# Kernel optimization log

Hardware: AMD Instinct MI355X
Metric: run time of the kernel (lower is better)

## Reference

```python
import jax, jax.numpy as jnp
import numpy as np

C = 128          # hidden width hard-coded in DirModelToFace
EPS = 1e-5       # BatchNorm1d eps


def sparse_bmm(rows, cols, vals, x, num_rows):
    """Batched sparse @ dense: COO (rows, cols, vals) shared across batch.
    x: [B, K, c] -> [B, num_rows, c]."""
    def one(xb):
        return jax.ops.segment_sum(xb[cols] * vals[:, None], rows, num_segments=num_rows)
    return jax.vmap(one)(x)


def conv1x1_prebn(x, gamma, beta, W, b):
    # GraphConv1x1(batch_norm='pre'): BN (training stats over B*N rows) then Linear
    mean = x.mean((0, 1))
    var = x.var((0, 1))  # biased, as torch BN uses for normalization
    xh = (x - mean) * jax.lax.rsqrt(var + EPS) * gamma + beta
    return xh @ W + b


def dir_block(Di, DiA, v, f, g, be, W, b):
    # DirResNet2 (res_f=False): quaternionic Dirac message passing
    B, N, _ = v.shape
    Fn = f.shape[1]
    msg_v = sparse_bmm(*DiA, f.reshape(B, 4 * Fn, C // 4), 4 * N).reshape(B, N, C)
    x = jax.nn.elu(jnp.concatenate([v, msg_v], axis=-1))
    v_out = v + conv1x1_prebn(x, g[0], be[0], W[0], b[0])
    msg_f = sparse_bmm(*Di, v_out.reshape(B, 4 * N, C // 4), 4 * Fn).reshape(B, Fn, C)
    x = jax.nn.elu(jnp.concatenate([f, msg_f], axis=-1))
    f_out = conv1x1_prebn(x, g[1], be[1], W[1], b[1])  # no residual on f
    return v_out, f_out


def avg_block(mask, v, g, be, W, b):
    # AvgResNet2: masked global average message
    x = v
    for j in range(2):
        x = jax.nn.elu(x)
        x_avg = (mask * x).sum(1, keepdims=True) / mask.sum(1, keepdims=True)
        x = jnp.concatenate([x, jnp.broadcast_to(x_avg, x.shape)], axis=-1)
        x = conv1x1_prebn(x, g[j], be[j], W[j], b[j])
    return x + v


def setup_inputs() -> dict:
    key = jax.random.key(0)
    ks = jax.random.split(key, 10)
    B, N, Fn = 4, 12000, 24000
    nnz = 48 * Fn  # 3 vertices per face x 4x4 quaternion block
    inputs = jax.random.normal(ks[0], (B, N, 3), jnp.float32)
    mask = jnp.ones((B, N, 1), jnp.float32)
    Di_rows = jax.random.randint(ks[1], (nnz,), 0, 4 * Fn, jnp.int32)
    Di_cols = jax.random.randint(ks[2], (nnz,), 0, 4 * N, jnp.int32)
    Di_vals = jax.random.normal(ks[3], (nnz,), jnp.float32) * 0.1
    DiA_rows = jax.random.randint(ks[4], (nnz,), 0, 4 * N, jnp.int32)
    DiA_cols = jax.random.randint(ks[5], (nnz,), 0, 4 * Fn, jnp.int32)
    DiA_vals = jax.random.normal(ks[6], (nnz,), jnp.float32) * 0.1
    W1 = jax.random.normal(ks[7], (3, C), jnp.float32) / np.sqrt(3.0)
    b1 = jnp.zeros((C,), jnp.float32)
    rn_gamma = jnp.ones((16, 2, 2 * C), jnp.float32)
    rn_beta = jnp.zeros((16, 2, 2 * C), jnp.float32)
    rn_W = jax.random.normal(ks[8], (16, 2, 2 * C, C), jnp.float32) / np.sqrt(2.0 * C)
    rn_b = jnp.zeros((16, 2, C), jnp.float32)
    g2 = jnp.ones((C,), jnp.float32)
    be2 = jnp.zeros((C,), jnp.float32)
    W2 = jax.random.normal(ks[9], (C, 1), jnp.float32) / np.sqrt(1.0 * C)
    b2 = jnp.zeros((1,), jnp.float32)
    return dict(inputs=inputs, mask=mask,
                Di_rows=Di_rows, Di_cols=Di_cols, Di_vals=Di_vals,
                DiA_rows=DiA_rows, DiA_cols=DiA_cols, DiA_vals=DiA_vals,
                W1=W1, b1=b1, rn_gamma=rn_gamma, rn_beta=rn_beta, rn_W=rn_W, rn_b=rn_b,
                g2=g2, be2=be2, W2=W2, b2=b2, num_faces=24000)


def reference(inputs, mask, Di_rows, Di_cols, Di_vals, DiA_rows, DiA_cols, DiA_vals,
              W1, b1, rn_gamma, rn_beta, rn_W, rn_b, g2, be2, W2, b2, num_faces):
    B, N, _ = inputs.shape
    v = inputs @ W1 + b1                       # conv1 (batch_norm=None)
    f = jnp.zeros((B, num_faces, C), v.dtype)  # face features start at zero
    Di = (Di_rows, Di_cols, Di_vals)
    DiA = (DiA_rows, DiA_cols, DiA_vals)
    for i in range(16):
        if i % 2 == 0:
            v, f = dir_block(Di, DiA, v, f, rn_gamma[i], rn_beta[i], rn_W[i], rn_b[i])
        else:
            v = avg_block(mask, v, rn_gamma[i], rn_beta[i], rn_W[i], rn_b[i])
    x = jax.nn.elu(f)
    return conv1x1_prebn(x, g2, be2, W2, b2)   # conv2 (batch_norm='pre')
```

## Files before the change

kernel.cpp:

```cpp
#include <hip/hip_runtime.h>
#include <hip/hip_fp16.h>
#include <math.h>


#define EPS 1e-5f

typedef float floatx4 __attribute__((ext_vector_type(4)));
typedef short shortx8 __attribute__((ext_vector_type(8)));

__device__ __forceinline__ float eluf(float x) { return x > 0.f ? x : expm1f(x); }
__device__ __forceinline__ float4 elu4(float4 v) {
    v.x = eluf(v.x); v.y = eluf(v.y); v.z = eluf(v.z); v.w = eluf(v.w); return v;
}
__device__ __forceinline__ short f2bf(float x) {
    unsigned u = __builtin_bit_cast(unsigned, x);
    u = u + 0x7FFFu + ((u >> 16) & 1u);
    return (short)(u >> 16);
}
__device__ __forceinline__ float bf2f(short h) {
    unsigned u = ((unsigned)(unsigned short)h) << 16;
    return __builtin_bit_cast(float, u);
}
__device__ __forceinline__ void split2(float x, short& hi, short& lo) {
    unsigned u = __builtin_bit_cast(unsigned, x);
    hi = (short)(u >> 16);
    float r = x - bf2f(hi);
    lo = (short)(__builtin_bit_cast(unsigned, r) >> 16);
}

__global__ void conv1_kernel(const float* __restrict__ in, const float* __restrict__ W1,
                             const float* __restrict__ b1, float* __restrict__ v,
                             __half* __restrict__ vH, int N, float* __restrict__ Sout,
                             const float* __restrict__ mask, float* __restrict__ msum,
                             int nConv) {
    __shared__ float sh[4];
    int t = threadIdx.x;
    if (blockIdx.x >= nConv) {
        int b = blockIdx.x - nConv;
        float s = 0.f;
        for (int n = t; n < N; n += 256) s += mask[(size_t)b * N + n];
        for (int o = 32; o > 0; o >>= 1) s += __shfl_down(s, o);
        if ((t & 63) == 0) sh[t >> 6] = s;
        __syncthreads();
        if (t == 0) msum[b] = sh[0] + sh[1] + sh[2] + sh[3];
        return;
    }
    int c = t & 127, half = t >> 7;
    int r0 = blockIdx.x * 64;
    float w0 = W1[c], w1 = W1[128 + c], w2 = W1[256 + c], bb = b1[c];
    float s1 = 0.f, s2 = 0.f;
    for (int k = 0; k < 32; ++k) {
        int r = r0 + half + 2 * k;
        float x0 = in[r * 3 + 0], x1 = in[r * 3 + 1], x2 = in[r * 3 + 2];
        float val = bb + x0 * w0 + x1 * w1 + x2 * w2;
        v[(size_t)r * 128 + c] = val;
        int b = r / N, vert = r - b * N;
        vH[(size_t)(4 * vert + (c >> 5)) * 128 + b * 32 + (c & 31)] = __float2half(val);
        float e = eluf(val);
        s1 += e; s2 += e * e;
    }
    atomicAdd(&Sout[c], s1);
    atomicAdd(&Sout[256 + c], s2);
}


__global__ void hist2_kernel(const int* __restrict__ rowsA, const int* __restrict__ rowsD,
                             int* __restrict__ cntA, int* __restrict__ cntD) {
    int e = blockIdx.x * 256 + threadIdx.x;
    if (blockIdx.y == 0) atomicAdd(&cntA[rowsA[e]], 1);
    else atomicAdd(&cntD[rowsD[e]], 1);
}

__global__ void partial2_kernel(const int* __restrict__ cntA, const int* __restrict__ cntD,
                                int* __restrict__ partA, int* __restrict__ partD,
                                int RA, int RD) {
    const int* counts = blockIdx.y ? cntD : cntA;
    int* partials = blockIdx.y ? partD : partA;
    int R = blockIdx.y ? RD : RA;
    int t = threadIdx.x;
    int base = blockIdx.x * 1024 + t * 4;
    int s = 0;
#pragma unroll
    for (int j = 0; j < 4; ++j) { int i = base + j; if (i < R) s += counts[i]; }
    __shared__ int sh[256];
    sh[t] = s; __syncthreads();
    for (int st = 128; st > 0; st >>= 1) {
        if (t < st) sh[t] += sh[t + st];
        __syncthreads();
    }
    if (t == 0) partials[blockIdx.x] = sh[0];
}

__global__ void scanp2_kernel(int* __restrict__ partA, int* __restrict__ partD,
                              int* __restrict__ ptrA, int* __restrict__ ptrD,
                              int PA, int PD, int RA, int RD, int total) {
    int* partials = blockIdx.y ? partD : partA;
    int* rowptr = blockIdx.y ? ptrD : ptrA;
    int P = blockIdx.y ? PD : PA;
    int R = blockIdx.y ? RD : RA;
    __shared__ int sh[256];
    int t = threadIdx.x;
    int v = (t < P) ? partials[t] : 0;
    sh[t] = v; __syncthreads();
    for (int st = 1; st < 256; st <<= 1) {
        int tmp = (t >= st) ? sh[t - st] : 0;
        __syncthreads();
        sh[t] += tmp;
        __syncthreads();
    }
    if (t < P) partials[t] = sh[t] - v;
    if (t == 0) rowptr[R] = total;
}

__global__ void apply2_kernel(int* __restrict__ cntA, int* __restrict__ cntD,
                              const int* __restrict__ partA, const int* __restrict__ partD,
                              int* __restrict__ ptrA, int* __restrict__ ptrD,
                              int RA, int RD) {
    int* counts = blockIdx.y ? cntD : cntA;
    const int* partials = blockIdx.y ? partD : partA;
    int* rowptr = blockIdx.y ? ptrD : ptrA;
    int R = blockIdx.y ? RD : RA;
    int t = threadIdx.x;
    int base = blockIdx.x * 1024 + t * 4;
    int c[4]; int s = 0;
#pragma unroll
    for (int j = 0; j < 4; ++j) { int i = base + j; c[j] = (i < R) ? counts[i] : 0; s += c[j]; }
    __shared__ int sh[256];
    sh[t] = s; __syncthreads();
    for (int st = 1; st < 256; st <<= 1) {
        int tmp = (t >= st) ? sh[t - st] : 0;
        __syncthreads();
        sh[t] += tmp;
        __syncthreads();
    }
    int off = partials[blockIdx.x] + sh[t] - s;
#pragma unroll
    for (int j = 0; j < 4; ++j) {
        int i = base + j;
        if (i < R) { rowptr[i] = off; counts[i] = off; }
        off += c[j];
    }
}

__global__ void scatter2_kernel(const int* __restrict__ rowsA, const int* __restrict__ colsA,
                                const float* __restrict__ valsA,
                                const int* __restrict__ rowsD, const int* __restrict__ colsD,
                                const float* __restrict__ valsD,
                                int* __restrict__ fillA, int* __restrict__ fillD,
                                int2* __restrict__ edgesA, int2* __restrict__ edgesD) {
    int e = blockIdx.x * 256 + threadIdx.x;
    if (blockIdx.y == 0) {
        int p = atomicAdd(&fillA[rowsA[e]], 1);
        edgesA[p] = make_int2(colsA[e], __float_as_int(valsA[e]));
    } else {
        int p = atomicAdd(&fillD[rowsD[e]], 1);
        edgesD[p] = make_int2(colsD[e], __float_as_int(valsD[e]));
    }
}

__global__ __launch_bounds__(1024) void spmm_csr_kernel(
    const int* __restrict__ rowptr, const int2* __restrict__ edges,
    const __half2* __restrict__ xH, float* __restrict__ y, int R4,
    float* __restrict__ Sout) {
    int t = threadIdx.x;
    int waveId = blockIdx.x * 16 + (t >> 6);
    int lane = t & 63;
    int b = lane >> 4, cp = lane & 15;
    const __half2* xb = xH + b * 16 + cp;
    size_t rs = (size_t)R4 * 32;
    __shared__ float red[256];
    if (t < 256) red[t] = 0.f;
    __syncthreads();
#pragma unroll
    for (int rr = 0; rr < 2; ++rr) {
        int r = waveId * 2 + rr;
        int e0 = rowptr[r], e1 = rowptr[r + 1];
        float ax = 0.f, ay = 0.f;
        int e = e0;
        for (; e + 4 <= e1; e += 4) {
            int2 E0 = edges[e], E1 = edges[e + 1], E2 = edges[e + 2], E3 = edges[e + 3];
            __half2 g0 = xb[(size_t)E0.x * 64];
            __half2 g1 = xb[(size_t)E1.x * 64];
            __half2 g2 = xb[(size_t)E2.x * 64];
            __half2 g3 = xb[(size_t)E3.x * 64];
            float v0 = __int_as_float(E0.y), v1 = __int_as_float(E1.y);
            float v2 = __int_as_float(E2.y), v3 = __int_as_float(E3.y);
            float2 f0 = __half22float2(g0), f1 = __half22float2(g1);
            float2 f2 = __half22float2(g2), f3 = __half22float2(g3);
            ax += v0 * f0.x; ay += v0 * f0.y;
            ax += v1 * f1.x; ay += v1 * f1.y;
            ax += v2 * f2.x; ay += v2 * f2.y;
            ax += v3 * f3.x; ay += v3 * f3.y;
        }
        for (; e < e1; ++e) {
            int2 E = edges[e];
            __half2 g = xb[(size_t)E.x * 64];
            float v = __int_as_float(E.y);
            float2 f = __half22float2(g);
            ax += v * f.x; ay += v * f.y;
        }
        *(float2*)&y[(size_t)b * rs + (size_t)r * 32 + cp * 2] = make_float2(ax, ay);
        float ea = eluf(ax), eb = eluf(ay);
        float s1a = ea, s2a = ea * ea, s1b = eb, s2b = eb * eb;
        s1a += __shfl_xor(s1a, 16); s1a += __shfl_xor(s1a, 32);
        s2a += __shfl_xor(s2a, 16); s2a += __shfl_xor(s2a, 32);
        s1b += __shfl_xor(s1b, 16); s1b += __shfl_xor(s1b, 32);
        s2b += __shfl_xor(s2b, 16); s2b += __shfl_xor(s2b, 32);
        if (lane < 16) {
            int ch = (r & 3) * 32 + cp * 2;
            atomicAdd(&red[ch], s1a);
            atomicAdd(&red[ch + 1], s1b);
            atomicAdd(&red[128 + ch], s2a);
            atomicAdd(&red[128 + ch + 1], s2b);
        }
    }
    __syncthreads();
    if (t < 128) atomicAdd(&Sout[128 + t], red[t]);
    else if (t < 256) atomicAdd(&Sout[384 + (t - 128)], red[t]);
}

__global__ __launch_bounds__(256) void gemm_mfma(
    const float* __restrict__ A, const float* __restrict__ Bs,
    const float* __restrict__ S, const float* __restrict__ gvec,
    const float* __restrict__ bevec, const float* __restrict__ Wfull,
    const float* __restrict__ bvec, const float* __restrict__ resid,
    float* __restrict__ out, __half* __restrict__ shadow,
    float* __restrict__ Sout, const float* __restrict__ mask,
    float* __restrict__ avgout, const float* __restrict__ avgacc,
    const float* __restrict__ msum, float invR,
    int rowsPerBatch, int modeB, int eluB) {
    __shared__ short Bsh[128 * 40];
    __shared__ short Bsl[128 * 40];
    __shared__ float sS[256];
    __shared__ float sMS[256];
    __shared__ float avgLDS[512];
    __shared__ float bparr[256];
    __shared__ float bpF[128];
    const int t = threadIdx.x;
    const int lane = t & 63;
    const int wave = t >> 6;
    const int rowBase = blockIdx.x * 128 + wave * 32;
    const int m = lane & 15;
    const int kq = lane >> 4;

    {
        int k = t;
        float mean, var;
        if (modeB == 1 && k >= 128) {
            int c = k - 128;
            float a0 = avgacc[c] / msum[0];
            float a1 = avgacc[128 + c] / msum[1];
            float a2 = avgacc[256 + c] / msum[2];
            float a3 = avgacc[384 + c] / msum[3];
            avgLDS[c] = a0; avgLDS[128 + c] = a1;
            avgLDS[256 + c] = a2; avgLDS[384 + c] = a3;
            mean = 0.25f * (a0 + a1 + a2 + a3);
            var = 0.25f * (a0 * a0 + a1 * a1 + a2 * a2 + a3 * a3) - mean * mean;
        } else {
            mean = S[k] * invR;
            var = S[256 + k] * invR - mean * mean;
        }
        float s = gvec[k] / sqrtf(var + EPS);
        sS[k] = s;
        sMS[k] = bevec[k] - mean * s;
    }

    floatx4 acc[2][8];
#pragma unroll
    for (int i = 0; i < 2; ++i)
#pragma unroll
        for (int j = 0; j < 8; ++j) acc[i][j] = {0.f, 0.f, 0.f, 0.f};

    float bpp0 = 0.f, bpp1 = 0.f;
    const int kbEnd = (modeB == 2) ? 4 : 8;
    for (int kb = 0; kb < kbEnd; ++kb) {
        const int k0 = kb * 32 + kq * 8;
        __syncthreads();
#pragma unroll
        for (int i = 0; i < 2; ++i) {
            int idx = t + 256 * i;
            int col = idx & 127, qs = idx >> 7;
            shortx8 hv, lv;
            float bps = 0.f;
#pragma unroll
            for (int j = 0; j < 8; ++j) {
                int k = kb * 32 + qs * 8 + j;
                float w = Wfull[(size_t)k * 128 + col];
                float wp = sS[k] * w;
                short h = f2bf(wp);
                hv[j] = h;
                lv[j] = f2bf(wp - bf2f(h));
                bps += sMS[k] * w;
            }
            *(shortx8*)&Bsh[col * 40 + qs * 8] = hv;
            *(shortx8*)&Bsl[col * 40 + qs * 8] = lv;
            if (i == 0) bpp0 += bps; else bpp1 += bps;
        }
        shortx8 ah[2], al[2];
#pragma unroll
        for (int rg = 0; rg < 2; ++rg) {
            int row = rowBase + rg * 16 + m;
            float4 p, q;
            if (kb < 4) {
                p = elu4(*(const float4*)&A[(size_t)row * 128 + k0]);
                q = elu4(*(const float4*)&A[(size_t)row * 128 + k0 + 4]);
            } else {
                int kk = k0 - 128;
                if (modeB == 0) {
                    p = *(const float4*)&Bs[(size_t)row * 128 + kk];
                    q = *(const float4*)&Bs[(size_t)row * 128 + kk + 4];
                    if (eluB) { p = elu4(p); q = elu4(q); }
                } else {
                    int b = row / rowsPerBatch;
                    p = *(const float4*)&avgLDS[b * 128 + kk];
                    q = *(const float4*)&avgLDS[b * 128 + kk + 4];
                }
            }
            float x[8] = {p.x, p.y, p.z, p.w, q.x, q.y, q.z, q.w};
#pragma unroll
            for (int j = 0; j < 8; ++j) {
                short h, l;
                split2(x[j], h, l);
                ah[rg][j] = h;
                al[rg][j] = l;
            }
        }
        __syncthreads();
#pragma unroll
        for (int ct = 0; ct < 8; ++ct) {
            int co = (ct * 16 + m) * 40 + kq * 8;
            shortx8 bh = *(const shortx8*)&Bsh[co];
            shortx8 bl = *(const shortx8*)&Bsl[co];
#pragma unroll
            for (int rg = 0; rg < 2; ++rg) {
                acc[rg][ct] = __builtin_amdgcn_mfma_f32_16x16x32_bf16(ah[rg], bh, acc[rg][ct], 0, 0, 0);
                acc[rg][ct] = __builtin_amdgcn_mfma_f32_16x16x32_bf16(ah[rg], bl, acc[rg][ct], 0, 0, 0);
                acc[rg][ct] = __builtin_amdgcn_mfma_f32_16x16x32_bf16(al[rg], bh, acc[rg][ct], 0, 0, 0);
            }
        }
    }
    if (modeB == 2) {
        int col = t & 127;
        float bps = 0.f;
        for (int j = 0; j < 64; ++j) {
            int k = 128 + (t >> 7) * 64 + j;
            bps += sMS[k] * Wfull[(size_t)k * 128 + col];
        }
        bpp0 += bps;
    }
    bparr[t] = bpp0 + bpp1;
    __syncthreads();
    if (t < 128) bpF[t] = bvec[t] + bparr[t] + bparr[t + 128];
    __syncthreads();

    const int bBlk = (blockIdx.x * 128) / rowsPerBatch;
    float mk8[8]; int ib8[8];
    if (avgout) {
#pragma unroll
        for (int rg = 0; rg < 2; ++rg)
#pragma unroll
            for (int r = 0; r < 4; ++r) {
                int row = rowBase + rg * 16 + kq * 4 + r;
                mk8[rg * 4 + r] = mask[row];
                ib8[rg * 4 + r] = (row >= (bBlk + 1) * rowsPerBatch) ? 1 : 0;
            }
    }
    float cs1[8], cs2[8], av0[8], av1[8];
#pragma unroll
    for (int ct = 0; ct < 8; ++ct) { cs1[ct] = 0.f; cs2[ct] = 0.f; av0[ct] = 0.f; av1[ct] = 0.f; }
#pragma unroll
    for (int ct = 0; ct < 8; ++ct) {
        int col = ct * 16 + m;
        float bb = bpF[col];
#pragma unroll
        for (int rg = 0; rg < 2; ++rg) {
#pragma unroll
            for (int r = 0; r < 4; ++r) {
                int row = rowBase + rg * 16 + kq * 4 + r;
                size_t o = (size_t)row * 128 + col;
                float v = acc[rg][ct][r] + bb;
                if (resid) v += resid[o];
                out[o] = v;
                if (shadow) {
                    int b = row / rowsPerBatch, vert = row - b * rowsPerBatch;
                    shadow[(size_t)(4 * vert + (col >> 5)) * 128 + b * 32 + (col & 31)] =
                        __float2half(v);
                }
                float e = eluf(v);
                cs1[ct] += e; cs2[ct] += e * e;
                if (avgout) {
                    float me = mk8[rg * 4 + r] * e;
                    if (ib8[rg * 4 + r]) av1[ct] += me; else av0[ct] += me;
                }
            }
        }
    }
    if (Sout) {
        __syncthreads();
        float* red = (float*)Bsh;
        float* redv = (float*)Bsl;
        red[t] = 0.f;
        if (avgout) redv[t] = 0.f;
        __syncthreads();
#pragma unroll
        for (int ct = 0; ct < 8; ++ct) {
            cs1[ct] += __shfl_xor(cs1[ct], 16); cs1[ct] += __shfl_xor(cs1[ct], 32);
            cs2[ct] += __shfl_xor(cs2[ct], 16); cs2[ct] += __shfl_xor(cs2[ct], 32);
            if (avgout) {
                av0[ct] += __shfl_xor(av0[ct], 16); av0[ct] += __shfl_xor(av0[ct], 32);
                av1[ct] += __shfl_xor(av1[ct], 16); av1[ct] += __shfl_xor(av1[ct], 32);
            }
        }
        if (kq == 0) {
#pragma unroll
            for (int ct = 0; ct < 8; ++ct) {
                atomicAdd(&red[ct * 16 + m], cs1[ct]);
                atomicAdd(&red[128 + ct * 16 + m], cs2[ct]);
                if (avgout) {
                    atomicAdd(&redv[ct * 16 + m], av0[ct]);
                    atomicAdd(&redv[128 + ct * 16 + m], av1[ct]);
                }
            }
        }
        __syncthreads();
        if (t < 128) atomicAdd(&Sout[t], red[t]);
        else atomicAdd(&Sout[256 + (t - 128)], red[t]);
        if (avgout) {
            int plane = t >> 7, col = t & 127;
            int b = bBlk + plane;
            if (b < 4) atomicAdd(&avgout[b * 128 + col], redv[t]);
        }
    }
}

__global__ void fold_final(const float* __restrict__ S, const float* __restrict__ g2,
                           const float* __restrict__ be2, const float* __restrict__ W2,
                           const float* __restrict__ b2, float* __restrict__ W2p, float invR) {
    __shared__ float red[128];
    int c = threadIdx.x;
    float mean = S[c] * invR;
    float var = S[256 + c] * invR - mean * mean;
    float s = g2[c] / sqrtf(var + EPS);
    float w = W2[c];
    W2p[c] = s * w;
    red[c] = (be2[c] - mean * s) * w;
    __syncthreads();
    for (int st = 64; st > 0; st >>= 1) {
        if (c < st) red[c] += red[c + st];
        __syncthreads();
    }
    if (c == 0) W2p[128] = b2[0] + red[0];
}

__global__ void final_out_kernel(const float* __restrict__ f, const float* __restrict__ W2p,
                                 float* __restrict__ out) {
    int t = threadIdx.x;
    int w = t >> 6, lane = t & 63;
    float wa = W2p[lane], wb = W2p[64 + lane], bb = W2p[128];
    int base = blockIdx.x * 16 + w * 4;
#pragma unroll
    for (int rr = 0; rr < 4; ++rr) {
        int row = base + rr;
        float a = eluf(f[(size_t)row * 128 + lane]) * wa +
                  eluf(f[(size_t)row * 128 + 64 + lane]) * wb;
        for (int off = 32; off > 0; off >>= 1) a += __shfl_down(a, off);
        if (lane == 0) out[row] = a + bb;
    }
}

extern "C" void kernel_launch(void* const* d_in, const int* in_sizes, int n_in,
                              void* d_out, int out_size, void* d_ws, size_t ws_size,
                              hipStream_t stream) {
    const float* inputs = (const float*)d_in[0];
    const float* mask = (const float*)d_in[1];
    const int* Di_rows = (const int*)d_in[2];
    const int* Di_cols = (const int*)d_in[3];
    const float* Di_vals = (const float*)d_in[4];
    const int* DiA_rows = (const int*)d_in[5];
    const int* DiA_cols = (const int*)d_in[6];
    const float* DiA_vals = (const float*)d_in[7];
    const float* W1 = (const float*)d_in[8];
    const float* b1 = (const float*)d_in[9];
    const float* rn_gamma = (const float*)d_in[10];
    const float* rn_beta = (const float*)d_in[11];
    const float* rn_W = (const float*)d_in[12];
    const float* rn_b = (const float*)d_in[13];
    const float* g2 = (const float*)d_in[14];
    const float* be2 = (const float*)d_in[15];
    const float* W2 = (const float*)d_in[16];
    const float* b2 = (const float*)d_in[17];
    float* out = (float*)d_out;

    const int B = 4;
    const int BN = in_sizes[1];
    const int N = BN / B;
    const int BF = out_size;
    const int Fn = BF / B;
    const int nnz = in_sizes[2];
    const int RA = 4 * N;
    const int RD = 4 * Fn;

    float* ws = (float*)d_ws;
    size_t off = 0;
    float* vA = ws + off;  off += (size_t)BN * 128;
    float* fA = ws + off;  off += (size_t)BF * 128;
    float* msg = ws + off; off += (size_t)BF * 128;
    __half* vH = (__half*)(ws + off); off += (size_t)RA * 128 / 2;
    __half* fH = (__half*)(ws + off); off += (size_t)RD * 128 / 2;
    int* ptrA    = (int*)(ws + off);  off += (size_t)RA + 4;
    int2* edgesA = (int2*)(ws + off); off += (size_t)nnz * 2;
    int* ptrD    = (int*)(ws + off);  off += (size_t)RD + 4;
    int2* edgesD = (int2*)(ws + off); off += (size_t)nnz * 2;
    int* cntA    = (int*)(ws + off);  off += (size_t)RA;
    int* cntD    = (int*)(ws + off);  off += (size_t)RD;
    int* partA   = (int*)(ws + off);  off += 256;
    int* partD   = (int*)(ws + off);  off += 256;
    float* Sarena = ws + off; off += 33 * 512;
    float* Aarena = ws + off; off += 16 * 512;
    float* msum = ws + off;   off += 4;
    float* W2p = ws + off; off += 132;

    const int eBlocks = nnz / 256;
    const int PA = (RA + 1023) / 1024;
    const int PD = (RD + 1023) / 1024;

    hipMemsetAsync(Sarena, 0, (33 * 512 + 16 * 512) * 4, stream);
    hipMemsetAsync(fA, 0, (size_t)BF * 128 * 4, stream);
    hipMemsetAsync(cntA, 0, (size_t)(RA + RD) * 4, stream);

    hist2_kernel<<<dim3(eBlocks, 2), 256, 0, stream>>>(DiA_rows, Di_rows, cntA, cntD);
    partial2_kernel<<<dim3(PD, 2), 256, 0, stream>>>(cntA, cntD, partA, partD, RA, RD);
    scanp2_kernel<<<dim3(1, 2), 256, 0, stream>>>(partA, partD, ptrA, ptrD, PA, PD,
                                                  RA, RD, nnz);
    apply2_kernel<<<dim3(PD, 2), 256, 0, stream>>>(cntA, cntD, partA, partD, ptrA, ptrD,
                                                   RA, RD);
    scatter2_kernel<<<dim3(eBlocks, 2), 256, 0, stream>>>(DiA_rows, DiA_cols, DiA_vals,
                                                          Di_rows, Di_cols, Di_vals,
                                                          cntA, cntD, edgesA, edgesD);

    auto slot = [&](int i, int j) { return Sarena + 512 * (2 * i + j); };
    float* Sfinal = Sarena + 512 * 32;

    conv1_kernel<<<BN / 64 + B, 256, 0, stream>>>(inputs, W1, b1, vA, vH, N, slot(0, 0),
                                                  mask, msum, BN / 64);

    for (int i = 0; i < 15; ++i) {
        if ((i & 1) == 0) {
            const float* g0 = rn_gamma + (size_t)(i * 2 + 0) * 256;
            const float* be0 = rn_beta + (size_t)(i * 2 + 0) * 256;
            const float* Wl0 = rn_W + (size_t)(i * 2 + 0) * 256 * 128;
            const float* bl0 = rn_b + (size_t)(i * 2 + 0) * 128;
            const float* g1 = rn_gamma + (size_t)(i * 2 + 1) * 256;
            const float* be1 = rn_beta + (size_t)(i * 2 + 1) * 256;
            const float* Wl1 = rn_W + (size_t)(i * 2 + 1) * 256 * 128;
            const float* bl1 = rn_b + (size_t)(i * 2 + 1) * 128;
            float* SoutV = (i < 14) ? slot(i + 1, 0) : nullptr;
            float* avgV = (i < 14) ? (Aarena + 512 * i) : nullptr;

            if (i == 0) {
                gemm_mfma<<<BN / 128, 256, 0, stream>>>(vA, nullptr, slot(0, 0), g0, be0,
                                                        Wl0, bl0, vA, vA, vH, SoutV, mask,
                                                        avgV, nullptr, nullptr, 1.f / BN,
                                                        N, 2, 1);
            } else {
                spmm_csr_kernel<<<RA / 32, 1024, 0, stream>>>(ptrA, edgesA,
                                                              (const __half2*)fH, msg, RA,
                                                              slot(i, 0));
                gemm_mfma<<<BN / 128, 256, 0, stream>>>(vA, msg, slot(i, 0), g0, be0,
                                                        Wl0, bl0, vA, vA, vH, SoutV, mask,
                                                        avgV, nullptr, nullptr, 1.f / BN,
                                                        N, 0, 1);
            }

            spmm_csr_kernel<<<RD / 32, 1024, 0, stream>>>(ptrD, edgesD, (const __half2*)vH,
                                                          msg, RD, slot(i, 1));
            gemm_mfma<<<BF / 128, 256, 0, stream>>>(fA, msg, slot(i, 1), g1, be1, Wl1, bl1,
                                                    nullptr, fA, fH,
                                                    (i < 14) ? slot(i + 2, 1) : Sfinal,
                                                    nullptr, nullptr, nullptr, nullptr,
                                                    1.f / BF, Fn, 0, 1);
        } else {
            for (int j = 0; j < 2; ++j) {
                const float* g = rn_gamma + (size_t)(i * 2 + j) * 256;
                const float* be = rn_beta + (size_t)(i * 2 + j) * 256;
                const float* Wlw = rn_W + (size_t)(i * 2 + j) * 256 * 128;
                const float* bl = rn_b + (size_t)(i * 2 + j) * 128;
                const float* src = (j == 0) ? vA : msg;
                float* dst = (j == 0) ? msg : vA;
                const float* resid = (j == 0) ? nullptr : vA;
                __half* shadow = (j == 0) ? nullptr : vH;
                float* SoutP = (j == 0) ? slot(i, 1) : slot(i + 1, 0);
                float* avgO = (j == 0) ? (Aarena + 512 * i) : nullptr;
                const float* avgacc = Aarena + 512 * (i - 1 + j);

                gemm_mfma<<<BN / 128, 256, 0, stream>>>(src, nullptr, slot(i, j), g, be,
                                                        Wlw, bl, resid, dst, shadow, SoutP,
                                                        mask, avgO, avgacc, msum,
                                                        1.f / BN, N, 1, 0);
            }
        }
    }

    fold_final<<<1, 128, 0, stream>>>(Sfinal, g2, be2, W2, b2, W2p, 1.f / BF);
    final_out_kernel<<<BF / 16, 256, 0, stream>>>(fA, W2p, out);
}
```

Baseline: 4.155 ms.

## Bucket CSR edges by column chunk and templatize gemm mode

The edge scatter into CSR now runs in several passes, each placing only edges whose column falls in one 8192-wide chunk. Within each row, edges therefore end up roughly ordered by column block, which should improve locality of the gathered half-precision rows in the SpMM. The gemm and spmm kernels also become templates on their mode, so per-mode branches resolve at compile time. The cost is extra scatter launches that each reread all edge arrays, plus more kernel instantiations.

```diff
diff --git a/kernel.cpp b/kernel.cpp
--- a/kernel.cpp
+++ b/kernel.cpp
@@ -147,17 +147,23 @@
                                 const int* __restrict__ rowsD, const int* __restrict__ colsD,
                                 const float* __restrict__ valsD,
                                 int* __restrict__ fillA, int* __restrict__ fillD,
-                                int2* __restrict__ edgesA, int2* __restrict__ edgesD) {
+                                int2* __restrict__ edgesA, int2* __restrict__ edgesD,
+                                int passA, int passD) {
     int e = blockIdx.x * 256 + threadIdx.x;
     if (blockIdx.y == 0) {
+        int c = colsA[e];
+        if ((c >> 13) != passA) return;
         int p = atomicAdd(&fillA[rowsA[e]], 1);
-        edgesA[p] = make_int2(colsA[e], __float_as_int(valsA[e]));
+        edgesA[p] = make_int2(c, __float_as_int(valsA[e]));
     } else {
+        int c = colsD[e];
+        if ((c >> 13) != passD) return;
         int p = atomicAdd(&fillD[rowsD[e]], 1);
-        edgesD[p] = make_int2(colsD[e], __float_as_int(valsD[e]));
-    }
-}
-
+        edgesD[p] = make_int2(c, __float_as_int(valsD[e]));
+    }
+}
+
+template <int DIR>
 __global__ __launch_bounds__(1024) void spmm_csr_kernel(
     const int* __restrict__ rowptr, const int2* __restrict__ edges,
     const __half2* __restrict__ xH, float* __restrict__ y, int R4,
@@ -219,6 +225,7 @@
     else if (t < 256) atomicAdd(&Sout[384 + (t - 128)], red[t]);
 }
 
+template <int MODEB>
 __global__ __launch_bounds__(256) void gemm_mfma(
     const float* __restrict__ A, const float* __restrict__ Bs,
     const float* __restrict__ S, const float* __restrict__ gvec,
@@ -227,8 +234,7 @@
     float* __restrict__ out, __half* __restrict__ shadow,
     float* __restrict__ Sout, const float* __restrict__ mask,
     float* __restrict__ avgout, const float* __restrict__ avgacc,
-    const float* __restrict__ msum, float invR,
-    int rowsPerBatch, int modeB, int eluB) {
+    const float* __restrict__ msum, float invR, int rowsPerBatch) {
     __shared__ short Bsh[128 * 40];
     __shared__ short Bsl[128 * 40];
     __shared__ float sS[256];
@@ -246,7 +252,7 @@
     {
         int k = t;
         float mean, var;
-        if (modeB == 1 && k >= 128) {
+        if (MODEB == 1 && k >= 128) {
             int c = k - 128;
             float a0 = avgacc[c] / msum[0];
             float a1 = avgacc[128 + c] / msum[1];
@@ -272,7 +278,7 @@
         for (int j = 0; j < 8; ++j) acc[i][j] = {0.f, 0.f, 0.f, 0.f};
 
     float bpp0 = 0.f, bpp1 = 0.f;
-    const int kbEnd = (modeB == 2) ? 4 : 8;
+    const int kbEnd = (MODEB == 2) ? 4 : 8;
     for (int kb = 0; kb < kbEnd; ++kb) {
         const int k0 = kb * 32 + kq * 8;
         __syncthreads();
@@ -306,10 +312,9 @@
                 q = elu4(*(const float4*)&A[(size_t)row * 128 + k0 + 4]);
             } else {
                 int kk = k0 - 128;
-                if (modeB == 0) {
-                    p = *(const float4*)&Bs[(size_t)row * 128 + kk];
-                    q = *(const float4*)&Bs[(size_t)row * 128 + kk + 4];
-                    if (eluB) { p = elu4(p); q = elu4(q); }
+                if (MODEB == 0) {
+                    p = elu4(*(const float4*)&Bs[(size_t)row * 128 + kk]);
+                    q = elu4(*(const float4*)&Bs[(size_t)row * 128 + kk + 4]);
                 } else {
                     int b = row / rowsPerBatch;
                     p = *(const float4*)&avgLDS[b * 128 + kk];
@@ -339,7 +344,7 @@
             }
         }
     }
-    if (modeB == 2) {
+    if (MODEB == 2) {
         int col = t & 127;
         float bps = 0.f;
         for (int j = 0; j < 64; ++j) {
@@ -534,9 +539,17 @@
                                                   RA, RD, nnz);
     apply2_kernel<<<dim3(PD, 2), 256, 0, stream>>>(cntA, cntD, partA, partD, ptrA, ptrD,
                                                    RA, RD);
-    scatter2_kernel<<<dim3(eBlocks, 2), 256, 0, stream>>>(DiA_rows, DiA_cols, DiA_vals,
-                                                          Di_rows, Di_cols, Di_vals,
-                                                          cntA, cntD, edgesA, edgesD);
+    {
+        const int chunksA = (4 * Fn + 8191) / 8192;
+        const int chunksD = (4 * N + 8191) / 8192;
+        const int passes = (chunksA > chunksD) ? chunksA : chunksD;
+        for (int p = 0; p < passes; ++p) {
+            scatter2_kernel<<<dim3(eBlocks, 2), 256, 0, stream>>>(
+                DiA_rows, DiA_cols, DiA_vals, Di_rows, Di_cols, Di_vals,
+                cntA, cntD, edgesA, edgesD,
+                (p < chunksA) ? p : -1, (p < chunksD) ? p : -1);
+        }
+    }
 
     auto slot = [&](int i, int j) { return Sarena + 512 * (2 * i + j); };
     float* Sfinal = Sarena + 512 * 32;
@@ -558,27 +571,28 @@
             float* avgV = (i < 14) ? (Aarena + 512 * i) : nullptr;
 
             if (i == 0) {
-                gemm_mfma<<<BN / 128, 256, 0, stream>>>(vA, nullptr, slot(0, 0), g0, be0,
-                                                        Wl0, bl0, vA, vA, vH, SoutV, mask,
-                                                        avgV, nullptr, nullptr, 1.f / BN,
-                                                        N, 2, 1);
+                gemm_mfma<2><<<BN / 128, 256, 0, stream>>>(vA, nullptr, slot(0, 0), g0, be0,
+                                                           Wl0, bl0, vA, vA, vH, SoutV, mask,
+                                                           avgV, nullptr, nullptr, 1.f / BN,
+                                                           N);
             } else {
-                spmm_csr_kernel<<<RA / 32, 1024, 0, stream>>>(ptrA, edgesA,
-                                                              (const __half2*)fH, msg, RA,
-                                                              slot(i, 0));
-                gemm_mfma<<<BN / 128, 256, 0, stream>>>(vA, msg, slot(i, 0), g0, be0,
-                                                        Wl0, bl0, vA, vA, vH, SoutV, mask,
-                                                        avgV, nullptr, nullptr, 1.f / BN,
-                                                        N, 0, 1);
-            }
-
-            spmm_csr_kernel<<<RD / 32, 1024, 0, stream>>>(ptrD, edgesD, (const __half2*)vH,
-                                                          msg, RD, slot(i, 1));
-            gemm_mfma<<<BF / 128, 256, 0, stream>>>(fA, msg, slot(i, 1), g1, be1, Wl1, bl1,
-                                                    nullptr, fA, fH,
-                                                    (i < 14) ? slot(i + 2, 1) : Sfinal,
-                                                    nullptr, nullptr, nullptr, nullptr,
-                                                    1.f / BF, Fn, 0, 1);
+                spmm_csr_kernel<0><<<RA / 32, 1024, 0, stream>>>(ptrA, edgesA,
+                                                                 (const __half2*)fH, msg,
+                                                                 RA, slot(i, 0));
+                gemm_mfma<0><<<BN / 128, 256, 0, stream>>>(vA, msg, slot(i, 0), g0, be0,
+                                                           Wl0, bl0, vA, vA, vH, SoutV, mask,
+                                                           avgV, nullptr, nullptr, 1.f / BN,
+                                                           N);
+            }
+
+            spmm_csr_kernel<1><<<RD / 32, 1024, 0, stream>>>(ptrD, edgesD,
+                                                             (const __half2*)vH, msg, RD,
+                                                             slot(i, 1));
+            gemm_mfma<0><<<BF / 128, 256, 0, stream>>>(fA, msg, slot(i, 1), g1, be1, Wl1,
+                                                       bl1, nullptr, fA, fH,
+                                                       (i < 14) ? slot(i + 2, 1) : Sfinal,
+                                                       nullptr, nullptr, nullptr, nullptr,
+                                                       1.f / BF, Fn);
         } else {
             for (int j = 0; j < 2; ++j) {
                 const float* g = rn_gamma + (size_t)(i * 2 + j) * 256;
@@ -593,10 +607,10 @@
                 float* avgO = (j == 0) ? (Aarena + 512 * i) : nullptr;
                 const float* avgacc = Aarena + 512 * (i - 1 + j);
 
-                gemm_mfma<<<BN / 128, 256, 0, stream>>>(src, nullptr, slot(i, j), g, be,
-                                                        Wlw, bl, resid, dst, shadow, SoutP,
-                                                        mask, avgO, avgacc, msum,
-                                                        1.f / BN, N, 1, 0);
+                gemm_mfma<1><<<BN / 128, 256, 0, stream>>>(src, nullptr, slot(i, j), g, be,
+                                                           Wlw, bl, resid, dst, shadow,
+                                                           SoutP, mask, avgO, avgacc, msum,
+                                                           1.f / BN, N);
             }
         }
     }
```

Measured after the change: 4.157 ms. Within noise of the previous version (+0.0%).
